# Performance work log

Hardware: AMD Instinct MI355X
Metric: run time of the kernel (lower is better)

## Reference

```python
import jax, jax.numpy as jnp
import numpy as np

N_DRUG, N_PROT = 20000, 8000
D_DRUG, D_PROT = 300, 1280
HIDDEN, OUT = 512, 5
N_EDGE, N_LBL = 500000, 200000


def setup_inputs() -> dict:
    key = jax.random.key(0)
    ks = jax.random.split(key, 12)
    inp = {
        "x_drug": jax.random.normal(ks[0], (N_DRUG, D_DRUG), dtype=jnp.float32),
        "x_prot": jax.random.normal(ks[1], (N_PROT, D_PROT), dtype=jnp.float32),
        "edge_src": jax.random.randint(ks[2], (N_EDGE,), 0, N_DRUG, dtype=jnp.int32),
        "edge_dst": jax.random.randint(ks[3], (N_EDGE,), 0, N_PROT, dtype=jnp.int32),
        "lbl_src": jax.random.randint(ks[4], (N_LBL,), 0, N_DRUG, dtype=jnp.int32),
        "lbl_dst": jax.random.randint(ks[5], (N_LBL,), 0, N_PROT, dtype=jnp.int32),
        # SAGEConv params: lin_l (on aggregated src msgs, with bias), lin_r (on dst, no bias)
        "W_l": jax.random.normal(ks[6], (HIDDEN, D_DRUG), dtype=jnp.float32) / np.sqrt(D_DRUG),
        "b_l": jnp.zeros((HIDDEN,), dtype=jnp.float32),
        "W_r": jax.random.normal(ks[7], (HIDDEN, D_PROT), dtype=jnp.float32) / np.sqrt(D_PROT),
        # final edge classifier Linear(D_DRUG + HIDDEN, OUT)
        "W_lin": jax.random.normal(ks[8], (OUT, D_DRUG + HIDDEN), dtype=jnp.float32) / np.sqrt(D_DRUG + HIDDEN),
        "b_lin": jnp.zeros((OUT,), dtype=jnp.float32),
    }
    return inp


def reference(x_drug, x_prot, edge_src, edge_dst, lbl_src, lbl_dst,
              W_l, b_l, W_r, W_lin, b_lin):
    # --- bipartite SAGEConv((drug, protein)) with default mean aggregation ---
    msg = x_drug[edge_src]                                   # [E, D_DRUG] gather
    agg = jax.ops.segment_sum(msg, edge_dst, num_segments=N_PROT)   # [N_PROT, D_DRUG]
    cnt = jax.ops.segment_sum(jnp.ones((edge_dst.shape[0],), jnp.float32),
                              edge_dst, num_segments=N_PROT)
    mean = agg / jnp.clip(cnt, 1.0, None)[:, None]           # mean over in-neighbors
    prot_emb_all = mean @ W_l.T + b_l + x_prot @ W_r.T       # [N_PROT, HIDDEN]

    # --- gather endpoints for labeled edges, concat, linear ---
    drug_emb = x_drug[lbl_src]                               # [L, D_DRUG]
    prot_emb = prot_emb_all[lbl_dst]                         # [L, HIDDEN]
    edge_emb = jnp.concatenate([drug_emb, prot_emb], axis=1) # [L, D_DRUG+HIDDEN]
    return edge_emb @ W_lin.T + b_lin                        # [L, OUT]
```

## Files before the change

kernel.cpp:

```cpp
#include <hip/hip_runtime.h>

#define N_DRUG 20000
#define N_PROT 8000
#define D_DRUG 300
#define D_PROT 1280
#define HIDDEN 512
#define OUT_D  5
#define N_EDGE 500000
#define N_LBL  200000
#define WLD    812
#define CAP    128
#define OVF_MAX 65536

__global__ void k_stage1(const float* __restrict__ W_l, const float* __restrict__ W_r,
                         const float* __restrict__ W_lin, const float* __restrict__ b_l,
                         const int* __restrict__ edge_src, const int* __restrict__ edge_dst,
                         float* __restrict__ A, float* __restrict__ B, float* __restrict__ c,
                         int* __restrict__ cnt, int* __restrict__ novf,
                         int* __restrict__ bucket, int* __restrict__ ovf) {
    int b = blockIdx.x;
    if (b < 248) {
        int t  = (b % 31) * 256 + threadIdx.x;
        int h0 = (b / 31) * 64;
        const int nA = OUT_D * D_DRUG;
        const int nB = OUT_D * D_PROT;
        if (t < nA) {
            int o = t / D_DRUG, k = t - o * D_DRUG;
            const float* wp = W_lin + o * WLD + D_DRUG + h0;
            const float* wl = W_l + (size_t)h0 * D_DRUG + k;
            float s = 0.f;
#pragma unroll 4
            for (int h = 0; h < 64; ++h) s += wp[h] * wl[h * D_DRUG];
            atomicAdd(&A[t], s);
        } else if (t < nA + nB) {
            int u = t - nA;
            int o = u / D_PROT, k = u - o * D_PROT;
            const float* wp = W_lin + o * WLD + D_DRUG + h0;
            const float* wr = W_r + (size_t)h0 * D_PROT + k;
            float s = 0.f;
#pragma unroll 4
            for (int h = 0; h < 64; ++h) s += wp[h] * wr[h * D_PROT];
            atomicAdd(&B[u], s);
        } else if (t < nA + nB + OUT_D) {
            int o = t - nA - nB;
            const float* wp = W_lin + o * WLD + D_DRUG + h0;
            float s = 0.f;
            for (int h = 0; h < 64; ++h) s += wp[h] * b_l[h0 + h];
            atomicAdd(&c[o], s);
        }
    } else {
        int base = (b - 248) * 2048 + threadIdx.x;
#pragma unroll
        for (int i = 0; i < 8; ++i) {
            int e = base + i * 256;
            if (e < N_EDGE) {
                int s = edge_src[e], d = edge_dst[e];
                int r = atomicAdd(&cnt[d], 1);
                if (r < CAP) {
                    bucket[d * CAP + r] = s;
                } else {
                    int o = atomicAdd(novf, 1);
                    if (o < OVF_MAX) { ovf[2 * o] = d; ovf[2 * o + 1] = s; }
                }
            }
        }
    }
}

__global__ void k_stage2(const float* __restrict__ x_drug, const float* __restrict__ x_prot,
                         const float* __restrict__ A, const float* __restrict__ B,
                         const float* __restrict__ c, const float* __restrict__ W_lin,
                         float* __restrict__ P_A, float* __restrict__ drugO,
                         float* __restrict__ protO) {
    int b = blockIdx.x;
    if (b < 1250) {
        int gid = b * 256 + threadIdx.x;
        int row = gid >> 4;
        int sub = threadIdx.x & 15;
        const float4* xr = (const float4*)(x_drug + (size_t)row * D_DRUG);
        float acc[10];
#pragma unroll
        for (int i = 0; i < 10; ++i) acc[i] = 0.f;
        for (int k = sub; k < D_DRUG / 4; k += 16) {
            float4 x = xr[k];
#pragma unroll
            for (int o = 0; o < OUT_D; ++o) {
                float4 a = ((const float4*)(A + o * D_DRUG))[k];
                acc[o] += x.x * a.x + x.y * a.y + x.z * a.z + x.w * a.w;
                float4 w = ((const float4*)(W_lin + o * WLD))[k];
                acc[5 + o] += x.x * w.x + x.y * w.y + x.z * w.z + x.w * w.w;
            }
        }
#pragma unroll
        for (int i = 0; i < 10; ++i) {
            float v = acc[i];
            for (int m = 8; m; m >>= 1) v += __shfl_xor(v, m, 64);
            acc[i] = v;
        }
        if (sub < OUT_D) {
            P_A[row * OUT_D + sub]   = acc[sub];
            drugO[row * OUT_D + sub] = acc[5 + sub];
        }
    } else {
        int wave = ((b - 1250) * 256 + threadIdx.x) >> 6;
        int lane = threadIdx.x & 63;
        const float4* xr = (const float4*)(x_prot + (size_t)wave * D_PROT);
        float acc[OUT_D] = {0.f, 0.f, 0.f, 0.f, 0.f};
        for (int k = lane; k < D_PROT / 4; k += 64) {
            float4 x = xr[k];
#pragma unroll
            for (int o = 0; o < OUT_D; ++o) {
                float4 bb = ((const float4*)(B + o * D_PROT))[k];
                acc[o] += x.x * bb.x + x.y * bb.y + x.z * bb.z + x.w * bb.w;
            }
        }
#pragma unroll
        for (int o = 0; o < OUT_D; ++o) {
            float v = acc[o];
            for (int off = 32; off; off >>= 1) v += __shfl_xor(v, off, 64);
            acc[o] = v;
        }
        if (lane < OUT_D) protO[wave * OUT_D + lane] = acc[lane] + c[lane];
    }
}

__global__ void k_gather(const int* __restrict__ cnt, const int* __restrict__ novf,
                         const int* __restrict__ bucket, const int* __restrict__ ovf,
                         const float* __restrict__ P_A, float* __restrict__ protO) {
    int wave = (blockIdx.x * blockDim.x + threadIdx.x) >> 6;
    int lane = threadIdx.x & 63;
    if (wave >= N_PROT) return;
    int deg = cnt[wave];
    int m = deg < CAP ? deg : CAP;
    float acc[OUT_D] = {0.f, 0.f, 0.f, 0.f, 0.f};
    const int* br = &bucket[wave * CAP];
    for (int j = lane; j < m; j += 64) {
        const float* p = &P_A[br[j] * OUT_D];
#pragma unroll
        for (int o = 0; o < OUT_D; ++o) acc[o] += p[o];
    }
    if (deg > CAP) {
        int nv = *novf; if (nv > OVF_MAX) nv = OVF_MAX;
        for (int j = lane; j < nv; j += 64) {
            if (ovf[2 * j] == wave) {
                const float* p = &P_A[ovf[2 * j + 1] * OUT_D];
#pragma unroll
                for (int o = 0; o < OUT_D; ++o) acc[o] += p[o];
            }
        }
    }
#pragma unroll
    for (int o = 0; o < OUT_D; ++o) {
        float v = acc[o];
        for (int off = 32; off; off >>= 1) v += __shfl_xor(v, off, 64);
        acc[o] = v;
    }
    if (lane < OUT_D)
        protO[wave * OUT_D + lane] += acc[lane] / fmaxf((float)deg, 1.f);
}

__global__ void k_final(const int* __restrict__ lbl_src, const int* __restrict__ lbl_dst,
                        const float* __restrict__ drugO, const float* __restrict__ protO,
                        const float* __restrict__ b_lin, float* __restrict__ out) {
    int l = blockIdx.x * blockDim.x + threadIdx.x;
    if (l >= N_LBL) return;
    int s = lbl_src[l], d = lbl_dst[l];
    const float* dr = &drugO[s * OUT_D];
    const float* pr = &protO[d * OUT_D];
    float* op = &out[(size_t)l * OUT_D];
    op[0] = dr[0] + pr[0] + b_lin[0];
    op[1] = dr[1] + pr[1] + b_lin[1];
    op[2] = dr[2] + pr[2] + b_lin[2];
    op[3] = dr[3] + pr[3] + b_lin[3];
    op[4] = dr[4] + pr[4] + b_lin[4];
}

extern "C" void kernel_launch(void* const* d_in, const int* in_sizes, int n_in,
                              void* d_out, int out_size, void* d_ws, size_t ws_size,
                              hipStream_t stream) {
    const float* x_drug   = (const float*)d_in[0];
    const float* x_prot   = (const float*)d_in[1];
    const int*   edge_src = (const int*)d_in[2];
    const int*   edge_dst = (const int*)d_in[3];
    const int*   lbl_src  = (const int*)d_in[4];
    const int*   lbl_dst  = (const int*)d_in[5];
    const float* W_l      = (const float*)d_in[6];
    const float* b_l      = (const float*)d_in[7];
    const float* W_r      = (const float*)d_in[8];
    const float* W_lin    = (const float*)d_in[9];
    const float* b_lin    = (const float*)d_in[10];
    float* out = (float*)d_out;

    char* ws = (char*)d_ws;
    int*   cnt    = (int*)  (ws + 0);
    int*   novf   = (int*)  (ws + 32000);
    float* A      = (float*)(ws + 32016);
    float* B      = (float*)(ws + 38016);
    float* c      = (float*)(ws + 63616);
    float* P_A    = (float*)(ws + 64000);
    float* drugO  = (float*)(ws + 464000);
    float* protO  = (float*)(ws + 864000);
    int*   bucket = (int*)  (ws + 1024000);
    int*   ovf    = (int*)  (ws + 5120000);

    hipMemsetAsync(ws, 0, 63648, stream);
    k_stage1<<<493, 256, 0, stream>>>(W_l, W_r, W_lin, b_l, edge_src, edge_dst,
                                      A, B, c, cnt, novf, bucket, ovf);
    k_stage2<<<3250, 256, 0, stream>>>(x_drug, x_prot, A, B, c, W_lin,
                                       P_A, drugO, protO);
    k_gather<<<(N_PROT * 64) / 256, 256, 0, stream>>>(cnt, novf, bucket, ovf, P_A, protO);
    k_final<<<(N_LBL + 255) / 256, 256, 0, stream>>>(lbl_src, lbl_dst, drugO, protO, b_lin, out);
}
```

Baseline: 166.0 us.

## Regroup stages: fold weights plus zeroing, then scatter overlapped with dense projections

Removes the memset by zeroing the counters inside the weight-folding kernel. The folding now uses 8 lanes per output joined by shuffle reductions instead of global atomics. The edge bucketing moves into the second kernel so it runs alongside the dense per-row projections. Per-protein counters are padded to a 128-byte stride to cut atomic contention on shared cache lines. The cost is a larger counter array to zero and a workspace layout that depends on fixed offsets.

```diff
diff --git a/kernel.cpp b/kernel.cpp
--- a/kernel.cpp
+++ b/kernel.cpp
@@ -11,51 +11,73 @@
 #define WLD    812
 #define CAP    128
 #define OVF_MAX 65536
-
-__global__ void k_stage1(const float* __restrict__ W_l, const float* __restrict__ W_r,
-                         const float* __restrict__ W_lin, const float* __restrict__ b_l,
-                         const int* __restrict__ edge_src, const int* __restrict__ edge_dst,
-                         float* __restrict__ A, float* __restrict__ B, float* __restrict__ c,
-                         int* __restrict__ cnt, int* __restrict__ novf,
-                         int* __restrict__ bucket, int* __restrict__ ovf) {
+#define CNT_STRIDE 32
+#define SCAT_B 245
+
+__global__ void k_fold_zero(const float* __restrict__ W_l, const float* __restrict__ W_r,
+                            const float* __restrict__ W_lin, const float* __restrict__ b_l,
+                            float* __restrict__ A, float* __restrict__ B, float* __restrict__ c,
+                            float4* __restrict__ cntz, int* __restrict__ novf) {
     int b = blockIdx.x;
     if (b < 248) {
-        int t  = (b % 31) * 256 + threadIdx.x;
-        int h0 = (b / 31) * 64;
+        int t  = b * 256 + threadIdx.x;
+        int e  = t >> 3;
+        int j  = t & 7;
+        int h0 = j * 64;
         const int nA = OUT_D * D_DRUG;
         const int nB = OUT_D * D_PROT;
-        if (t < nA) {
-            int o = t / D_DRUG, k = t - o * D_DRUG;
+        float s = 0.f;
+        if (e < nA) {
+            int o = e / D_DRUG, k = e - o * D_DRUG;
             const float* wp = W_lin + o * WLD + D_DRUG + h0;
-            const float* wl = W_l + (size_t)h0 * D_DRUG + k;
-            float s = 0.f;
-#pragma unroll 4
-            for (int h = 0; h < 64; ++h) s += wp[h] * wl[h * D_DRUG];
-            atomicAdd(&A[t], s);
-        } else if (t < nA + nB) {
-            int u = t - nA;
+            const float* w  = W_l + (size_t)h0 * D_DRUG + k;
+#pragma unroll 8
+            for (int h = 0; h < 64; ++h) s += wp[h] * w[h * D_DRUG];
+        } else if (e < nA + nB) {
+            int u = e - nA;
             int o = u / D_PROT, k = u - o * D_PROT;
             const float* wp = W_lin + o * WLD + D_DRUG + h0;
-            const float* wr = W_r + (size_t)h0 * D_PROT + k;
-            float s = 0.f;
-#pragma unroll 4
-            for (int h = 0; h < 64; ++h) s += wp[h] * wr[h * D_PROT];
-            atomicAdd(&B[u], s);
-        } else if (t < nA + nB + OUT_D) {
-            int o = t - nA - nB;
+            const float* w  = W_r + (size_t)h0 * D_PROT + k;
+#pragma unroll 8
+            for (int h = 0; h < 64; ++h) s += wp[h] * w[h * D_PROT];
+        } else if (e < nA + nB + OUT_D) {
+            int o = e - nA - nB;
             const float* wp = W_lin + o * WLD + D_DRUG + h0;
-            float s = 0.f;
+#pragma unroll 8
             for (int h = 0; h < 64; ++h) s += wp[h] * b_l[h0 + h];
-            atomicAdd(&c[o], s);
+        }
+        s += __shfl_xor(s, 1, 64);
+        s += __shfl_xor(s, 2, 64);
+        s += __shfl_xor(s, 4, 64);
+        if (j == 0) {
+            if (e < nA)                     A[e] = s;
+            else if (e < nA + nB)           B[e - nA] = s;
+            else if (e < nA + nB + OUT_D)   c[e - nA - nB] = s;
         }
     } else {
-        int base = (b - 248) * 2048 + threadIdx.x;
+        int idx = (b - 248) * 256 + threadIdx.x;
+        cntz[idx] = make_float4(0.f, 0.f, 0.f, 0.f);
+        if (idx == 0) *novf = 0;
+    }
+}
+
+__global__ void k_scatter_dense(const float* __restrict__ x_drug, const float* __restrict__ x_prot,
+                                const int* __restrict__ edge_src, const int* __restrict__ edge_dst,
+                                const float* __restrict__ A, const float* __restrict__ B,
+                                const float* __restrict__ c, const float* __restrict__ W_lin,
+                                int* __restrict__ cnt, int* __restrict__ novf,
+                                int* __restrict__ bucket, int* __restrict__ ovf,
+                                float* __restrict__ P_A, float* __restrict__ drugO,
+                                float* __restrict__ protO) {
+    int b = blockIdx.x;
+    if (b < SCAT_B) {
+        int base = b * 2048 + threadIdx.x;
 #pragma unroll
         for (int i = 0; i < 8; ++i) {
             int e = base + i * 256;
             if (e < N_EDGE) {
                 int s = edge_src[e], d = edge_dst[e];
-                int r = atomicAdd(&cnt[d], 1);
+                int r = atomicAdd(&cnt[d * CNT_STRIDE], 1);
                 if (r < CAP) {
                     bucket[d * CAP + r] = s;
                 } else {
@@ -64,17 +86,8 @@
                 }
             }
         }
-    }
-}
-
-__global__ void k_stage2(const float* __restrict__ x_drug, const float* __restrict__ x_prot,
-                         const float* __restrict__ A, const float* __restrict__ B,
-                         const float* __restrict__ c, const float* __restrict__ W_lin,
-                         float* __restrict__ P_A, float* __restrict__ drugO,
-                         float* __restrict__ protO) {
-    int b = blockIdx.x;
-    if (b < 1250) {
-        int gid = b * 256 + threadIdx.x;
+    } else if (b < SCAT_B + 1250) {
+        int gid = (b - SCAT_B) * 256 + threadIdx.x;
         int row = gid >> 4;
         int sub = threadIdx.x & 15;
         const float4* xr = (const float4*)(x_drug + (size_t)row * D_DRUG);
@@ -102,7 +115,7 @@
             drugO[row * OUT_D + sub] = acc[5 + sub];
         }
     } else {
-        int wave = ((b - 1250) * 256 + threadIdx.x) >> 6;
+        int wave = ((b - SCAT_B - 1250) * 256 + threadIdx.x) >> 6;
         int lane = threadIdx.x & 63;
         const float4* xr = (const float4*)(x_prot + (size_t)wave * D_PROT);
         float acc[OUT_D] = {0.f, 0.f, 0.f, 0.f, 0.f};
@@ -130,7 +143,7 @@
     int wave = (blockIdx.x * blockDim.x + threadIdx.x) >> 6;
     int lane = threadIdx.x & 63;
     if (wave >= N_PROT) return;
-    int deg = cnt[wave];
+    int deg = cnt[wave * CNT_STRIDE];
     int m = deg < CAP ? deg : CAP;
     float acc[OUT_D] = {0.f, 0.f, 0.f, 0.f, 0.f};
     const int* br = &bucket[wave * CAP];
@@ -193,21 +206,21 @@
 
     char* ws = (char*)d_ws;
     int*   cnt    = (int*)  (ws + 0);
-    int*   novf   = (int*)  (ws + 32000);
-    float* A      = (float*)(ws + 32016);
-    float* B      = (float*)(ws + 38016);
-    float* c      = (float*)(ws + 63616);
-    float* P_A    = (float*)(ws + 64000);
-    float* drugO  = (float*)(ws + 464000);
-    float* protO  = (float*)(ws + 864000);
-    int*   bucket = (int*)  (ws + 1024000);
-    int*   ovf    = (int*)  (ws + 5120000);
-
-    hipMemsetAsync(ws, 0, 63648, stream);
-    k_stage1<<<493, 256, 0, stream>>>(W_l, W_r, W_lin, b_l, edge_src, edge_dst,
-                                      A, B, c, cnt, novf, bucket, ovf);
-    k_stage2<<<3250, 256, 0, stream>>>(x_drug, x_prot, A, B, c, W_lin,
-                                       P_A, drugO, protO);
-    k_gather<<<(N_PROT * 64) / 256, 256, 0, stream>>>(cnt, novf, bucket, ovf, P_A, protO);
+    int*   novf   = (int*)  (ws + 1048576);
+    float* A      = (float*)(ws + 1048592);
+    float* B      = (float*)(ws + 1054592);
+    float* c      = (float*)(ws + 1080192);
+    float* P_A    = (float*)(ws + 1080320);
+    float* drugO  = (float*)(ws + 1480320);
+    float* protO  = (float*)(ws + 1880320);
+    int*   bucket = (int*)  (ws + 2040320);
+    int*   ovf    = (int*)  (ws + 6136320);
+
+    k_fold_zero<<<504, 256, 0, stream>>>(W_l, W_r, W_lin, b_l, A, B, c,
+                                         (float4*)cnt, novf);
+    k_scatter_dense<<<3495, 256, 0, stream>>>(x_drug, x_prot, edge_src, edge_dst,
+                                              A, B, c, W_lin, cnt, novf, bucket, ovf,
+                                              P_A, drugO, protO);
+    k_gather<<<2000, 256, 0, stream>>>(cnt, novf, bucket, ovf, P_A, protO);
     k_final<<<(N_LBL + 255) / 256, 256, 0, stream>>>(lbl_src, lbl_dst, drugO, protO, b_lin, out);
 }
```

After: 164.5 us. About the same (-0.9%).
